# Optimization experiments

Measured on AMD Instinct MI355X. Metric: run time of the kernel, lower is better.

## Reference

```python
import jax, jax.numpy as jnp
import numpy as np

N_NODES = 50000
N_EDGES = 1600000
N_FEAT = 128
EMB = 128
N_CLASSES = 10
N_GRAPHS = 512


def setup_inputs() -> dict:
    key = jax.random.key(0)
    ks = jax.random.split(key, 12)
    x = jax.random.normal(ks[0], (N_NODES, N_FEAT), dtype=jnp.float32)
    edge_index = jax.random.randint(ks[1], (2, N_EDGES), 0, N_NODES, dtype=jnp.int64)
    batch = jnp.sort(jax.random.randint(ks[2], (N_NODES,), 0, N_GRAPHS, dtype=jnp.int64))
    def glorot(k, fan_in, fan_out):
        lim = jnp.sqrt(6.0 / (fan_in + fan_out)).astype(jnp.float32)
        return jax.random.uniform(k, (fan_in, fan_out), jnp.float32, -lim, lim)
    W0 = glorot(ks[3], N_FEAT, EMB); b0 = jnp.zeros((EMB,), jnp.float32)
    W1 = glorot(ks[4], EMB, EMB);    b1 = jnp.zeros((EMB,), jnp.float32)
    W2 = glorot(ks[5], EMB, EMB);    b2 = jnp.zeros((EMB,), jnp.float32)
    Wout = glorot(ks[6], EMB, N_CLASSES)
    bout = jnp.zeros((N_CLASSES,), jnp.float32)
    return {"x": x, "edge_index": edge_index, "batch": batch,
            "W0": W0, "b0": b0, "W1": W1, "b1": b1, "W2": W2, "b2": b2,
            "Wout": Wout, "bout": bout}


def _gcn_conv(x, W, b, src, dst, norm, n_nodes):
    # PyG GCNConv: h = x @ W; aggregate norm * h[src] into dst; add bias.
    h = x @ W                                  # [N, out]
    msg = h[src] * norm[:, None]               # [E+N, out] gather (incl. self-loops)
    out = jax.ops.segment_sum(msg, dst, num_segments=n_nodes)
    return out + b


def reference(x, edge_index, batch, W0, b0, W1, b1, W2, b2, Wout, bout):
    n_nodes = x.shape[0]
    # add self-loops (GCNConv default add_self_loops=True)
    loops = jnp.arange(n_nodes, dtype=edge_index.dtype)
    src = jnp.concatenate([edge_index[0], loops])
    dst = jnp.concatenate([edge_index[1], loops])
    # symmetric normalization D^{-1/2} (A+I) D^{-1/2}
    deg = jax.ops.segment_sum(jnp.ones_like(dst, dtype=x.dtype), dst,
                              num_segments=n_nodes)
    deg_inv_sqrt = jnp.where(deg > 0, jax.lax.rsqrt(jnp.maximum(deg, 1.0)), 0.0)
    norm = deg_inv_sqrt[src] * deg_inv_sqrt[dst]   # [E+N]
    out = jnp.tanh(_gcn_conv(x, W0, b0, src, dst, norm, n_nodes))
    out = jnp.tanh(_gcn_conv(out, W1, b1, src, dst, norm, n_nodes))
    out = _gcn_conv(out, W2, b2, src, dst, norm, n_nodes)
    # global mean pool over per-node graph ids
    sums = jax.ops.segment_sum(out, batch, num_segments=N_GRAPHS)
    counts = jax.ops.segment_sum(jnp.ones((n_nodes,), out.dtype), batch,
                                 num_segments=N_GRAPHS)
    pooled = sums / jnp.maximum(counts, 1.0)[:, None]   # [G, EMB]
    logits = pooled @ Wout + bout                        # [G, C]
    return jax.nn.log_softmax(logits, axis=1)
```

## Files before the change

### kernel.cpp

```cpp
#include <hip/hip_runtime.h>
#include <math.h>


#define BLK_EDGES 4096
#define MAXB 128
#define ECAP 4096
#define NPB 8
#define WS_STRIDE 136

typedef __attribute__((ext_vector_type(8))) short bf16x8;
typedef __attribute__((ext_vector_type(4))) float f32x4;
typedef __attribute__((ext_vector_type(2))) float f32x2;

static __device__ inline unsigned short f2bf(float f) {
    unsigned u = __float_as_uint(f);
    unsigned r = (u + 0x7FFFu + ((u >> 16) & 1u)) >> 16;
    return (unsigned short)r;
}
static __device__ inline float bf_lo(unsigned u) { return __uint_as_float(u << 16); }
static __device__ inline float bf_hi(unsigned u) { return __uint_as_float(u & 0xFFFF0000u); }
static __device__ inline unsigned char f2fp8(float v) {
    v = fminf(fmaxf(v, -240.f), 240.f);
    int u = __builtin_amdgcn_cvt_pk_fp8_f32(v, v, 0, false);
    return (unsigned char)(u & 0xFF);
}
static __device__ inline float fast_tanh(float x) {
    float ax = fabsf(x);
    float e = __expf(2.0f * ax);
    float r = fmaf(-2.0f, __builtin_amdgcn_rcpf(e + 1.0f), 1.0f);
    return copysignf(r, x);
}

__global__ __launch_bounds__(256) void blk_hist_prep(const int* __restrict__ dst,
        int* __restrict__ histT, int E, int NBLK, int NB,
        const float* __restrict__ W0, const float* __restrict__ W1,
        const float* __restrict__ W2, unsigned short* __restrict__ wt0,
        unsigned short* __restrict__ wt1, unsigned short* __restrict__ wt2,
        unsigned char* __restrict__ hs, int N) {
    __shared__ int h[MAXB];
    int blk = blockIdx.x, t = threadIdx.x;
    if (blk >= NBLK) {
        if (blk == NBLK && t < 32)
            ((unsigned*)(hs + (size_t)N * 128))[t] = 0u;
        int i = (blk - NBLK) * 256 + t;
        int w = i >> 14, j = i & 16383;
        int k = j >> 7, n2 = j & 127;
        const float* Wp = (w == 0) ? W0 : (w == 1) ? W1 : W2;
        unsigned short* Wt = (w == 0) ? wt0 : (w == 1) ? wt1 : wt2;
        Wt[n2 * 128 + k] = f2bf(Wp[k * 128 + n2]);
        return;
    }
    for (int i = t; i < NB; i += 256) h[i] = 0;
    __syncthreads();
    int lo = blk * BLK_EDGES;
    int hi = min(E, lo + BLK_EDGES);
    for (int i = lo + t; i < hi; i += 256)
        atomicAdd(&h[dst[i] >> 9], 1);
    __syncthreads();
    for (int i = t; i < NB; i += 256) histT[i * NBLK + blk] = h[i];
}

__global__ void scan_block(const int* __restrict__ cnt, int* __restrict__ off,
                           int* __restrict__ bsum, int n) {
    __shared__ int lds[256];
    int t = threadIdx.x;
    int i = blockIdx.x * 256 + t;
    int v = (i < n) ? cnt[i] : 0;
    lds[t] = v;
    __syncthreads();
    for (int d = 1; d < 256; d <<= 1) {
        int add = (t >= d) ? lds[t - d] : 0;
        __syncthreads();
        lds[t] += add;
        __syncthreads();
    }
    if (i < n) off[i] = lds[t] - v;
    if (t == 255) bsum[blockIdx.x] = lds[255];
}

__global__ void scan_top(const int* __restrict__ bsum, int* __restrict__ boff,
                         int nblocks) {
    __shared__ int lds[256];
    int t = threadIdx.x;
    int v = (t < nblocks) ? bsum[t] : 0;
    lds[t] = v;
    __syncthreads();
    for (int d = 1; d < 256; d <<= 1) {
        int add = (t >= d) ? lds[t - d] : 0;
        __syncthreads();
        lds[t] += add;
        __syncthreads();
    }
    if (t < nblocks) boff[t] = lds[t] - v;
}

__global__ __launch_bounds__(256) void scatter_packed(const int* __restrict__ src,
        const int* __restrict__ dst, const int* __restrict__ P,
        const int* __restrict__ boff, unsigned* __restrict__ packed,
        int E, int NBLK, int NB) {
    __shared__ int cur[MAXB];
    int blk = blockIdx.x, t = threadIdx.x;
    for (int i = t; i < NB; i += 256) {
        int idx = i * NBLK + blk;
        cur[i] = P[idx] + boff[idx >> 8];
    }
    __syncthreads();
    int lo = blk * BLK_EDGES;
    int hi = min(E, lo + BLK_EDGES);
    for (int i = lo + t; i < hi; i += 256) {
        int d = dst[i];
        int pos = atomicAdd(&cur[d >> 9], 1);
        packed[pos] = ((unsigned)d << 16) | (unsigned)src[i];
    }
}

__global__ __launch_bounds__(256) void bucket_build(const unsigned* __restrict__ packed,
        const int* __restrict__ P, const int* __restrict__ boff, int* __restrict__ off,
        float* __restrict__ dis, unsigned short* __restrict__ csr16,
        int E, int NBLK, int N, int NB) {
    __shared__ int cnt[512];
    __shared__ int loc[512];
    __shared__ int ps[256];
    int b = blockIdx.x, t = threadIdx.x;
    int i0 = b * NBLK, i1 = (b + 1) * NBLK;
    int start = P[i0] + boff[i0 >> 8];
    int end   = (b == NB - 1) ? E : (P[i1] + boff[i1 >> 8]);
    cnt[t] = 0; cnt[t + 256] = 0;
    __syncthreads();
    for (int i = start + t; i < end; i += 256)
        atomicAdd(&cnt[(packed[i] >> 16) & 511], 1);
    __syncthreads();
    int c0 = cnt[2 * t], c1 = cnt[2 * t + 1];
    ps[t] = c0 + c1;
    __syncthreads();
    for (int d = 1; d < 256; d <<= 1) {
        int add = (t >= d) ? ps[t - d] : 0;
        __syncthreads();
        ps[t] += add;
        __syncthreads();
    }
    int pexcl = ps[t] - (c0 + c1);
    loc[2 * t]     = start + pexcl;
    loc[2 * t + 1] = start + pexcl + c0;
    __syncthreads();
    int node0 = b * 512;
    for (int l = t; l < 512; l += 256) {
        int node = node0 + l;
        if (node < N) {
            off[node] = loc[l];
            dis[node] = rsqrtf((float)cnt[l] + 1.0f);
        }
    }
    if (b == NB - 1 && t == 0) off[N] = E;
    __syncthreads();
    for (int i = start + t; i < end; i += 256) {
        unsigned p = packed[i];
        int l = (p >> 16) & 511;
        int pos = atomicAdd(&loc[l], 1);
        csr16[pos] = (unsigned short)(p & 0xFFFFu);
    }
}

template<int IN_F32>
__global__ __launch_bounds__(256) void gemm_mfma(const void* __restrict__ Av,
        const unsigned short* __restrict__ Wt, const float* __restrict__ dis,
        unsigned char* __restrict__ Hs8, int n) {
    __shared__ unsigned short Ws[128 * WS_STRIDE];
    int t = threadIdx.x;
    for (int i = t; i < 128 * 16; i += 256) {
        int r = i >> 4, j = i & 15;
        uint4 u = ((const uint4*)(Wt + r * 128))[j];
        int pr = ((r & 7) << 4) | (r >> 3);
        *(uint4*)&Ws[pr * WS_STRIDE + j * 8] = u;
    }
    __syncthreads();

    int wave = t >> 6, lane = t & 63;
    int quad = lane >> 4, l16 = lane & 15;
    int row0 = blockIdx.x * 128 + wave * 32;

    int ra0 = row0 + l16;      if (ra0 >= n) ra0 = n - 1;
    int ra1 = row0 + 16 + l16; if (ra1 >= n) ra1 = n - 1;

    f32x4 acc[2][8];
    const f32x4 z = {0.f, 0.f, 0.f, 0.f};
#pragma unroll
    for (int mi = 0; mi < 2; ++mi)
#pragma unroll
        for (int ni = 0; ni < 8; ++ni) acc[mi][ni] = z;

#pragma unroll
    for (int ks = 0; ks < 4; ++ks) {
        int kof = ks * 32 + quad * 8;
        bf16x8 a0, a1;
        if (IN_F32) {
            const float* A0 = (const float*)Av + (size_t)ra0 * 128 + kof;
            const float* A1 = (const float*)Av + (size_t)ra1 * 128 + kof;
            float4 p0 = ((const float4*)A0)[0], p1 = ((const float4*)A0)[1];
            float4 q0 = ((const float4*)A1)[0], q1 = ((const float4*)A1)[1];
            a0[0] = (short)f2bf(p0.x); a0[1] = (short)f2bf(p0.y);
            a0[2] = (short)f2bf(p0.z); a0[3] = (short)f2bf(p0.w);
            a0[4] = (short)f2bf(p1.x); a0[5] = (short)f2bf(p1.y);
            a0[6] = (short)f2bf(p1.z); a0[7] = (short)f2bf(p1.w);
            a1[0] = (short)f2bf(q0.x); a1[1] = (short)f2bf(q0.y);
            a1[2] = (short)f2bf(q0.z); a1[3] = (short)f2bf(q0.w);
            a1[4] = (short)f2bf(q1.x); a1[5] = (short)f2bf(q1.y);
            a1[6] = (short)f2bf(q1.z); a1[7] = (short)f2bf(q1.w);
        } else {
            a0 = *(const bf16x8*)((const unsigned short*)Av + (size_t)ra0 * 128 + kof);
            a1 = *(const bf16x8*)((const unsigned short*)Av + (size_t)ra1 * 128 + kof);
        }
        bf16x8 b[8];
#pragma unroll
        for (int ni = 0; ni < 8; ++ni)
            b[ni] = *(const bf16x8*)&Ws[(ni * 16 + l16) * WS_STRIDE + kof];
#pragma unroll
        for (int ni = 0; ni < 8; ++ni) {
            acc[0][ni] = __builtin_amdgcn_mfma_f32_16x16x32_bf16(a0, b[ni], acc[0][ni], 0, 0, 0);
            acc[1][ni] = __builtin_amdgcn_mfma_f32_16x16x32_bf16(a1, b[ni], acc[1][ni], 0, 0, 0);
        }
    }
#pragma unroll
    for (int mi = 0; mi < 2; ++mi) {
        int rb = row0 + mi * 16 + quad * 4;
#pragma unroll
        for (int reg = 0; reg < 4; ++reg) {
            int r = rb + reg;
            if (r < n) {
                float dv = dis[r];
                float v[8];
#pragma unroll
                for (int ni = 0; ni < 8; ++ni)
                    v[ni] = fminf(fmaxf(acc[mi][ni][reg] * dv, -240.f), 240.f);
                int d0 = __builtin_amdgcn_cvt_pk_fp8_f32(v[0], v[1], 0, false);
                d0 = __builtin_amdgcn_cvt_pk_fp8_f32(v[2], v[3], d0, true);
                int d1 = __builtin_amdgcn_cvt_pk_fp8_f32(v[4], v[5], 0, false);
                d1 = __builtin_amdgcn_cvt_pk_fp8_f32(v[6], v[7], d1, true);
                uint2 o; o.x = (unsigned)d0; o.y = (unsigned)d1;
                *(uint2*)(Hs8 + (size_t)r * 128 + l16 * 8) = o;
            }
        }
    }
}

template<int DO_TANH>
__global__ __launch_bounds__(512) void aggregate3(const unsigned char* __restrict__ hs,
    const unsigned short* __restrict__ csr, const int* __restrict__ off,
    const float* __restrict__ dis, const float* __restrict__ bias,
    unsigned* __restrict__ outp, int n) {
    __shared__ unsigned short eidx[ECAP + 16];
    int t = threadIdx.x;
    int node0 = blockIdx.x * NPB;
    int b0 = off[node0];
    int top = node0 + NPB < n ? node0 + NPB : n;
    int bN = off[top];
    int mblk = bN - b0;
    bool staged = (mblk <= ECAP);
    if (staged)
        for (int i = t; i < mblk; i += 512) eidx[i] = csr[b0 + i];
    __syncthreads();

    int node = node0 + (t >> 6);
    if (node >= n) return;
    int lane = t & 63;
    int g = lane >> 4;
    int fq = lane & 15;
    unsigned fob = (unsigned)fq << 3;

    int e0 = off[node];
    int e1 = off[node + 1];
    int le0 = e0 - b0;
    int m = e1 - e0;

    unsigned sv = *(const unsigned short*)(hs + (((unsigned)node) << 7) + fob + 2 * g);

    const f32x2 z2 = {0.f, 0.f};
    f32x2 c01 = z2, c23 = z2, c45 = z2, c67 = z2;
    auto cadd = [&](uint2 v) {
        c01 += __builtin_amdgcn_cvt_pk_f32_fp8((int)v.x, false);
        c23 += __builtin_amdgcn_cvt_pk_f32_fp8((int)v.x, true);
        c45 += __builtin_amdgcn_cvt_pk_f32_fp8((int)v.y, false);
        c67 += __builtin_amdgcn_cvt_pk_f32_fp8((int)v.y, true);
    };
    uint2 va[4], vb[4];
    auto sumB = [&](uint2* v) {
#pragma unroll
        for (int j = 0; j < 4; ++j) cadd(v[j]);
    };
    auto loadL = [&](int i, uint2* v) {
#pragma unroll
        for (int j = 0; j < 4; ++j) {
            int e = i + g + 4 * j;
            int idx = eidx[le0 + e];
            idx = (e < m) ? idx : n;
            v[j] = *(const uint2*)(hs + ((unsigned)idx << 7) + fob);
        }
    };
    auto loadG = [&](int i, uint2* v) {
#pragma unroll
        for (int j = 0; j < 4; ++j) {
            int e = i + g + 4 * j;
            int idx = csr[e0 + e];
            idx = (e < m) ? idx : n;
            v[j] = *(const uint2*)(hs + ((unsigned)idx << 7) + fob);
        }
    };

    int B = (m + 15) >> 4;
    if (B) {
        if (staged) {
            loadL(0, va);
            int k = 1;
            for (; k + 1 < B; k += 2) {
                loadL(k << 4, vb);       sumB(va);
                loadL((k + 1) << 4, va); sumB(vb);
            }
            if (k < B) { loadL(k << 4, vb); sumB(va); sumB(vb); }
            else       { sumB(va); }
        } else {
            loadG(0, va);
            int k = 1;
            for (; k + 1 < B; k += 2) {
                loadG(k << 4, vb);       sumB(va);
                loadG((k + 1) << 4, va); sumB(vb);
            }
            if (k < B) { loadG(k << 4, vb); sumB(va); sumB(vb); }
            else       { sumB(va); }
        }
    }

    float a0 = c01.x, a1 = c01.y, a2 = c23.x, a3 = c23.y;
    float a4 = c45.x, a5 = c45.y, a6 = c67.x, a7 = c67.y;

    a0 += __shfl_xor(a0, 32, 64); a0 += __shfl_xor(a0, 16, 64);
    a1 += __shfl_xor(a1, 32, 64); a1 += __shfl_xor(a1, 16, 64);
    a2 += __shfl_xor(a2, 32, 64); a2 += __shfl_xor(a2, 16, 64);
    a3 += __shfl_xor(a3, 32, 64); a3 += __shfl_xor(a3, 16, 64);
    a4 += __shfl_xor(a4, 32, 64); a4 += __shfl_xor(a4, 16, 64);
    a5 += __shfl_xor(a5, 32, 64); a5 += __shfl_xor(a5, 16, 64);
    a6 += __shfl_xor(a6, 32, 64); a6 += __shfl_xor(a6, 16, 64);
    a7 += __shfl_xor(a7, 32, 64); a7 += __shfl_xor(a7, 16, 64);

    float s0 = (g & 2) ? ((g & 1) ? a6 : a4) : ((g & 1) ? a2 : a0);
    float s1 = (g & 2) ? ((g & 1) ? a7 : a5) : ((g & 1) ? a3 : a1);
    f32x2 sf = __builtin_amdgcn_cvt_pk_f32_fp8((int)sv, false);
    s0 += sf.x;
    s1 += sf.y;
    float dn = dis[node];
    float2 bv = ((const float2*)bias)[fq * 4 + g];
    float o0 = fmaf(dn, s0, bv.x);
    float o1 = fmaf(dn, s1, bv.y);
    if (DO_TANH) { o0 = fast_tanh(o0); o1 = fast_tanh(o1); }
    unsigned o = (unsigned)f2bf(o0) | ((unsigned)f2bf(o1) << 16);
    outp[(size_t)node * 64 + fq * 4 + g] = o;
}

__global__ __launch_bounds__(256) void pool_head(const unsigned* __restrict__ actb,
    const int* __restrict__ batch, const float* __restrict__ Wout,
    const float* __restrict__ bout, float* __restrict__ out, int n, int C) {
    __shared__ float psum[4][128];
    __shared__ float l[16];
    __shared__ float stats[2];
    int g = blockIdx.x;
    int t = threadIdx.x;
    int w = t >> 6;
    int lane = t & 63;
    int lo = 0, hi = n;
    while (lo < hi) { int mid = (lo + hi) >> 1; if (batch[mid] < g) lo = mid + 1; else hi = mid; }
    int lo1 = lo, hi1 = n;
    while (lo1 < hi1) { int mid = (lo1 + hi1) >> 1; if (batch[mid] < g + 1) lo1 = mid + 1; else hi1 = mid; }
    float ax = 0.f, ay = 0.f;
    for (int i = lo + w; i < lo1; i += 4) {
        unsigned v = actb[(size_t)i * 64 + lane];
        ax += bf_lo(v);
        ay += bf_hi(v);
    }
    psum[w][2 * lane]     = ax;
    psum[w][2 * lane + 1] = ay;
    __syncthreads();
    if (w == 0) {
        int cnt = lo1 - lo;
        float inv = 1.0f / (float)(cnt > 0 ? cnt : 1);
        float sx = (psum[0][2 * lane] + psum[1][2 * lane])
                 + (psum[2][2 * lane] + psum[3][2 * lane]);
        float sy = (psum[0][2 * lane + 1] + psum[1][2 * lane + 1])
                 + (psum[2][2 * lane + 1] + psum[3][2 * lane + 1]);
        psum[0][2 * lane]     = sx * inv;
        psum[0][2 * lane + 1] = sy * inv;
    }
    __syncthreads();
    if (t < C) {
        float acc = bout[t];
        for (int f = 0; f < 128; ++f)
            acc = fmaf(psum[0][f], Wout[(size_t)f * C + t], acc);
        l[t] = acc;
    }
    __syncthreads();
    if (t == 0) {
        float m = -1e30f;
        for (int c = 0; c < C; ++c) m = fmaxf(m, l[c]);
        float s = 0.f;
        for (int c = 0; c < C; ++c) s += expf(l[c] - m);
        stats[0] = m;
        stats[1] = logf(s);
    }
    __syncthreads();
    if (t < C) out[(size_t)g * C + t] = l[t] - stats[0] - stats[1];
}

extern "C" void kernel_launch(void* const* d_in, const int* in_sizes, int n_in,
                              void* d_out, int out_size, void* d_ws, size_t ws_size,
                              hipStream_t stream) {
    const float* x     = (const float*)d_in[0];
    const int*   edge  = (const int*)d_in[1];
    const int*   batch = (const int*)d_in[2];
    const float* W0 = (const float*)d_in[3];
    const float* b0 = (const float*)d_in[4];
    const float* W1 = (const float*)d_in[5];
    const float* b1 = (const float*)d_in[6];
    const float* W2 = (const float*)d_in[7];
    const float* b2 = (const float*)d_in[8];
    const float* Wout = (const float*)d_in[9];
    const float* bout = (const float*)d_in[10];
    float* out = (float*)d_out;

    const int N = in_sizes[0] / 128;
    const int E = in_sizes[1] / 2;
    const int C = in_sizes[10];
    const int G = out_size / C;

    const int* src = edge;
    const int* dst = edge + E;

    const int NBLK = (E + BLK_EDGES - 1) / BLK_EDGES;
    const int NB   = (N + 511) / 512;
    const int NBQ  = NB * NBLK;
    const int PREPB = (3 * 16384) / 256;

    char* p = (char*)d_ws;
    auto alloc = [&](size_t bytes) -> void* {
        void* r = (void*)p;
        p += (bytes + 255) & ~(size_t)255;
        return r;
    };
    unsigned char* hs = (unsigned char*)alloc((size_t)(N + 1) * 128);
    unsigned* actb = (unsigned*)alloc((size_t)N * 128 * 2);
    float* dis    = (float*)alloc((size_t)N * 4);
    int*   off    = (int*)alloc((size_t)(N + 1) * 4);
    int*   P      = (int*)alloc((size_t)(NBQ + 1) * 4);
    int*   bsum   = (int*)alloc(256 * 4);
    int*   boff   = (int*)alloc(256 * 4);
    unsigned* packed = (unsigned*)alloc((size_t)E * 4);
    unsigned short* csr16 = (unsigned short*)alloc((size_t)(E + 16) * 2);
    unsigned short* wt0 = (unsigned short*)alloc(128 * 128 * 2);
    unsigned short* wt1 = (unsigned short*)alloc(128 * 128 * 2);
    unsigned short* wt2 = (unsigned short*)alloc(128 * 128 * 2);

    const int sb = (NBQ + 255) / 256;

    blk_hist_prep<<<NBLK + PREPB, 256, 0, stream>>>(dst, P, E, NBLK, NB,
                                                    W0, W1, W2, wt0, wt1, wt2,
                                                    hs, N);
    scan_block<<<sb, 256, 0, stream>>>(P, P, bsum, NBQ);
    scan_top<<<1, 256, 0, stream>>>(bsum, boff, sb);
    scatter_packed<<<NBLK, 256, 0, stream>>>(src, dst, P, boff, packed, E, NBLK, NB);
    bucket_build<<<NB, 256, 0, stream>>>(packed, P, boff, off, dis, csr16, E, NBLK, N, NB);

    const int gb = (N + 127) / 128;
    const int ab = (N + NPB - 1) / NPB;

    gemm_mfma<1><<<gb, 256, 0, stream>>>(x,    wt0, dis, hs, N);
    aggregate3<1><<<ab, 512, 0, stream>>>(hs, csr16, off, dis, b0, actb, N);
    gemm_mfma<0><<<gb, 256, 0, stream>>>(actb, wt1, dis, hs, N);
    aggregate3<1><<<ab, 512, 0, stream>>>(hs, csr16, off, dis, b1, actb, N);
    gemm_mfma<0><<<gb, 256, 0, stream>>>(actb, wt2, dis, hs, N);
    aggregate3<0><<<ab, 512, 0, stream>>>(hs, csr16, off, dis, b2, actb, N);

    pool_head<<<G, 256, 0, stream>>>(actb, batch, Wout, bout, out, N, C);
}
```

Measured before the change: 294.5 us.

## Split GCN aggregation into two feature-half passes over the neighbor gather

Each aggregation launch is replaced by two launches, each handling 64 of the 128 fp8 feature bytes per node. Within a wave, 8 lanes cover a node's half-row and 8 edge groups run in parallel, with an extra shuffle stage to reduce across them. The aim is to halve the gathered working set per pass so neighbor rows are more likely to stay in cache. In exchange, CSR indices are read twice, there are more launches, and rows are gathered at 64-byte granularity.

After: 364.6 us. +23.8%, slower.

```diff
diff --git a/kernel.cpp b/kernel.cpp
--- a/kernel.cpp
+++ b/kernel.cpp
@@ -247,7 +247,7 @@
 __global__ __launch_bounds__(512) void aggregate3(const unsigned char* __restrict__ hs,
     const unsigned short* __restrict__ csr, const int* __restrict__ off,
     const float* __restrict__ dis, const float* __restrict__ bias,
-    unsigned* __restrict__ outp, int n) {
+    unsigned* __restrict__ outp, int n, int h) {
     __shared__ unsigned short eidx[ECAP + 16];
     int t = threadIdx.x;
     int node0 = blockIdx.x * NPB;
@@ -263,16 +263,16 @@
     int node = node0 + (t >> 6);
     if (node >= n) return;
     int lane = t & 63;
-    int g = lane >> 4;
-    int fq = lane & 15;
-    unsigned fob = (unsigned)fq << 3;
+    int g = lane >> 3;
+    int fq = lane & 7;
+    unsigned fob = (unsigned)(h * 64 + fq * 8);
 
     int e0 = off[node];
     int e1 = off[node + 1];
     int le0 = e0 - b0;
     int m = e1 - e0;
 
-    unsigned sv = *(const unsigned short*)(hs + (((unsigned)node) << 7) + fob + 2 * g);
+    unsigned sv = *(const unsigned short*)(hs + (((unsigned)node) << 7) + fob + 2 * (g & 3));
 
     const f32x2 z2 = {0.f, 0.f};
     f32x2 c01 = z2, c23 = z2, c45 = z2, c67 = z2;
@@ -282,15 +282,14 @@
         c45 += __builtin_amdgcn_cvt_pk_f32_fp8((int)v.y, false);
         c67 += __builtin_amdgcn_cvt_pk_f32_fp8((int)v.y, true);
     };
-    uint2 va[4], vb[4];
+    uint2 va[2], vb[2];
     auto sumB = [&](uint2* v) {
-#pragma unroll
-        for (int j = 0; j < 4; ++j) cadd(v[j]);
+        cadd(v[0]); cadd(v[1]);
     };
     auto loadL = [&](int i, uint2* v) {
 #pragma unroll
-        for (int j = 0; j < 4; ++j) {
-            int e = i + g + 4 * j;
+        for (int j = 0; j < 2; ++j) {
+            int e = i + g + 8 * j;
             int idx = eidx[le0 + e];
             idx = (e < m) ? idx : n;
             v[j] = *(const uint2*)(hs + ((unsigned)idx << 7) + fob);
@@ -298,8 +297,8 @@
     };
     auto loadG = [&](int i, uint2* v) {
 #pragma unroll
-        for (int j = 0; j < 4; ++j) {
-            int e = i + g + 4 * j;
+        for (int j = 0; j < 2; ++j) {
+            int e = i + g + 8 * j;
             int idx = csr[e0 + e];
             idx = (e < m) ? idx : n;
             v[j] = *(const uint2*)(hs + ((unsigned)idx << 7) + fob);
@@ -332,27 +331,29 @@
     float a0 = c01.x, a1 = c01.y, a2 = c23.x, a3 = c23.y;
     float a4 = c45.x, a5 = c45.y, a6 = c67.x, a7 = c67.y;
 
-    a0 += __shfl_xor(a0, 32, 64); a0 += __shfl_xor(a0, 16, 64);
-    a1 += __shfl_xor(a1, 32, 64); a1 += __shfl_xor(a1, 16, 64);
-    a2 += __shfl_xor(a2, 32, 64); a2 += __shfl_xor(a2, 16, 64);
-    a3 += __shfl_xor(a3, 32, 64); a3 += __shfl_xor(a3, 16, 64);
-    a4 += __shfl_xor(a4, 32, 64); a4 += __shfl_xor(a4, 16, 64);
-    a5 += __shfl_xor(a5, 32, 64); a5 += __shfl_xor(a5, 16, 64);
-    a6 += __shfl_xor(a6, 32, 64); a6 += __shfl_xor(a6, 16, 64);
-    a7 += __shfl_xor(a7, 32, 64); a7 += __shfl_xor(a7, 16, 64);
-
-    float s0 = (g & 2) ? ((g & 1) ? a6 : a4) : ((g & 1) ? a2 : a0);
-    float s1 = (g & 2) ? ((g & 1) ? a7 : a5) : ((g & 1) ? a3 : a1);
-    f32x2 sf = __builtin_amdgcn_cvt_pk_f32_fp8((int)sv, false);
-    s0 += sf.x;
-    s1 += sf.y;
-    float dn = dis[node];
-    float2 bv = ((const float2*)bias)[fq * 4 + g];
-    float o0 = fmaf(dn, s0, bv.x);
-    float o1 = fmaf(dn, s1, bv.y);
-    if (DO_TANH) { o0 = fast_tanh(o0); o1 = fast_tanh(o1); }
-    unsigned o = (unsigned)f2bf(o0) | ((unsigned)f2bf(o1) << 16);
-    outp[(size_t)node * 64 + fq * 4 + g] = o;
+    a0 += __shfl_xor(a0, 32, 64); a0 += __shfl_xor(a0, 16, 64); a0 += __shfl_xor(a0, 8, 64);
+    a1 += __shfl_xor(a1, 32, 64); a1 += __shfl_xor(a1, 16, 64); a1 += __shfl_xor(a1, 8, 64);
+    a2 += __shfl_xor(a2, 32, 64); a2 += __shfl_xor(a2, 16, 64); a2 += __shfl_xor(a2, 8, 64);
+    a3 += __shfl_xor(a3, 32, 64); a3 += __shfl_xor(a3, 16, 64); a3 += __shfl_xor(a3, 8, 64);
+    a4 += __shfl_xor(a4, 32, 64); a4 += __shfl_xor(a4, 16, 64); a4 += __shfl_xor(a4, 8, 64);
+    a5 += __shfl_xor(a5, 32, 64); a5 += __shfl_xor(a5, 16, 64); a5 += __shfl_xor(a5, 8, 64);
+    a6 += __shfl_xor(a6, 32, 64); a6 += __shfl_xor(a6, 16, 64); a6 += __shfl_xor(a6, 8, 64);
+    a7 += __shfl_xor(a7, 32, 64); a7 += __shfl_xor(a7, 16, 64); a7 += __shfl_xor(a7, 8, 64);
+
+    if (g < 4) {
+        float s0 = (g & 2) ? ((g & 1) ? a6 : a4) : ((g & 1) ? a2 : a0);
+        float s1 = (g & 2) ? ((g & 1) ? a7 : a5) : ((g & 1) ? a3 : a1);
+        f32x2 sf = __builtin_amdgcn_cvt_pk_f32_fp8((int)sv, false);
+        s0 += sf.x;
+        s1 += sf.y;
+        float dn = dis[node];
+        float2 bv = ((const float2*)bias)[h * 32 + fq * 4 + g];
+        float o0 = fmaf(dn, s0, bv.x);
+        float o1 = fmaf(dn, s1, bv.y);
+        if (DO_TANH) { o0 = fast_tanh(o0); o1 = fast_tanh(o1); }
+        unsigned o = (unsigned)f2bf(o0) | ((unsigned)f2bf(o1) << 16);
+        outp[(size_t)node * 64 + h * 32 + fq * 4 + g] = o;
+    }
 }
 
 __global__ __launch_bounds__(256) void pool_head(const unsigned* __restrict__ actb,
@@ -470,11 +471,14 @@
     const int ab = (N + NPB - 1) / NPB;
 
     gemm_mfma<1><<<gb, 256, 0, stream>>>(x,    wt0, dis, hs, N);
-    aggregate3<1><<<ab, 512, 0, stream>>>(hs, csr16, off, dis, b0, actb, N);
+    aggregate3<1><<<ab, 512, 0, stream>>>(hs, csr16, off, dis, b0, actb, N, 0);
+    aggregate3<1><<<ab, 512, 0, stream>>>(hs, csr16, off, dis, b0, actb, N, 1);
     gemm_mfma<0><<<gb, 256, 0, stream>>>(actb, wt1, dis, hs, N);
-    aggregate3<1><<<ab, 512, 0, stream>>>(hs, csr16, off, dis, b1, actb, N);
+    aggregate3<1><<<ab, 512, 0, stream>>>(hs, csr16, off, dis, b1, actb, N, 0);
+    aggregate3<1><<<ab, 512, 0, stream>>>(hs, csr16, off, dis, b1, actb, N, 1);
     gemm_mfma<0><<<gb, 256, 0, stream>>>(actb, wt2, dis, hs, N);
-    aggregate3<0><<<ab, 512, 0, stream>>>(hs, csr16, off, dis, b2, actb, N);
+    aggregate3<0><<<ab, 512, 0, stream>>>(hs, csr16, off, dis, b2, actb, N, 0);
+    aggregate3<0><<<ab, 512, 0, stream>>>(hs, csr16, off, dis, b2, actb, N, 1);
 
     pool_head<<<G, 256, 0, stream>>>(actb, batch, Wout, bout, out, N, C);
 }
```
